# Kernel tuning notes

Hardware: AMD Instinct MI355X
Metric: run time of the kernel (lower is better)

The kernel has to match this reference:

```python
import jax, jax.numpy as jnp
import numpy as np

B, N, C, Cn, M = 4, 4096, 32, 64, 64


def fps(event, npoint):
    """Farthest point sampling, faithful to farthest_point_sample_batch.
    Returns selected points in ORIGINAL index order (masked_select semantics).
    event: [B, n, c] -> [B, npoint, c]
    """
    b, n, c = event.shape
    bidx = jnp.arange(b)
    barycenter = jnp.mean(event, axis=1, keepdims=True)            # [B,1,c]
    d0 = jnp.sum((event - barycenter) ** 2, axis=-1)               # [B,n]
    farthest = jnp.argmax(d0, axis=1)                              # [B]
    distance = jnp.full((b, n), 1e10, dtype=event.dtype)
    sel = jnp.zeros((b, n), dtype=bool)

    def body(carry, _):
        distance, farthest, sel = carry
        sel = sel.at[bidx, farthest].set(True)
        centroid = jnp.take_along_axis(event, farthest[:, None, None], axis=1)  # [B,1,c]
        d = jnp.sum((event - centroid) ** 2, axis=-1)              # [B,n]
        distance = jnp.minimum(distance, d)
        farthest = jnp.argmax(distance, axis=1)
        return (distance, farthest, sel), None

    (distance, farthest, sel), _ = jax.lax.scan(
        body, (distance, farthest, sel), None, length=npoint)
    # masked_select keeps original index order: stable sort puts selected first
    order = jnp.argsort(~sel, axis=1, stable=True)[:, :npoint]     # [B,npoint]
    return jnp.take_along_axis(event, order[:, :, None], axis=1)   # [B,npoint,c]


def setup_inputs() -> dict:
    key = jax.random.key(0)
    ks = jax.random.split(key, 7)
    s = 0.1
    return {
        "events_feature": jax.random.normal(ks[0], (B, N, C), jnp.float32),
        "W_qs": jax.random.normal(ks[1], (Cn, C), jnp.float32) * s,
        "W_ks": jax.random.normal(ks[2], (Cn, C), jnp.float32) * s,
        "W_vs": jax.random.normal(ks[3], (Cn, C), jnp.float32) * s,
        "W_pe": jax.random.normal(ks[4], (Cn, C), jnp.float32) * s,
        "W_sa1": jax.random.normal(ks[5], (1, Cn), jnp.float32) * s,
        "W_sa2": jax.random.normal(ks[6], (C, Cn), jnp.float32) * s,
    }


def reference(events_feature, W_qs, W_ks, W_vs, W_pe, W_sa1, W_sa2):
    q = events_feature @ W_qs.T                                   # [B,N,Cn]
    k = events_feature @ W_ks.T                                   # [B,N,Cn]
    v = events_feature @ W_vs.T                                   # [B,N,Cn]

    # position encoding: pairwise diff to M FPS-sampled events, then C->Cn
    ev_m = fps(events_feature, M)                                 # [B,M,C]
    pe = events_feature[:, :, None, :] - ev_m[:, None, :, :]      # [B,N,M,C]
    pe = pe @ W_pe.T                                              # [B,N,M,Cn]

    k_m = fps(k, M)                                               # [B,M,Cn]
    v_m = fps(v, M)                                               # [B,M,Cn]

    # vector attention scores: (q - k_m + pe) -> scalar per (n,m)
    sa = q[:, :, None, :] - k_m[:, None, :, :] + pe               # [B,N,M,Cn]
    logits = jnp.squeeze(sa @ W_sa1.T, -1)                        # [B,N,M]
    scores = jax.nn.softmax(logits, axis=-1)                      # [B,N,M]

    # Original: matmul(scores[B,1,N,M], (v_multi+pe).permute->[B,Cn,M,N]) then
    # sum over last axis. Summing first over n' is the same math and avoids the
    # [B,Cn,N,N] intermediate: sum_{n'} v_multi = N * v_m; sum_{n'} pe.
    S = N * v_m + jnp.sum(pe, axis=1)                             # [B,M,Cn]
    attn = jnp.einsum('bnm,bmc->bnc', scores, S)                  # [B,N,Cn]
    return attn @ W_sa2.T                                         # [B,N,C]
```

## Files before the change

kernel.cpp:

```cpp
#include <hip/hip_runtime.h>

constexpr int N_ = 4096, C_ = 32, CN_ = 64, M_ = 64;
constexpr int TPB = 1024;
constexpr int RPT = 3, LPT = 1;
constexpr int NREG = RPT * TPB;
constexpr int NLDS = N_ - NREG;
constexpr int NWAVES = TPB / 64;
constexpr int NTPB = 256;
constexpr int NCHUNK = N_ / NTPB;

__device__ __forceinline__ void pkfma(float2& a, float x0, float x1,
                                      float y0, float y1) {
  a.x = fmaf(x0, y0, a.x);
  a.y = fmaf(x1, y1, a.y);
}

__device__ __forceinline__ unsigned long long shfl_xor_u64(unsigned long long v, int m) {
  unsigned lo = __shfl_xor((unsigned)v, m);
  unsigned hi = __shfl_xor((unsigned)(v >> 32), m);
  return ((unsigned long long)hi << 32) | lo;
}

__device__ __forceinline__ unsigned fmap(float v) {
  unsigned u = __float_as_uint(v);
  u ^= (unsigned)((int)u >> 31) | 0x80000000u;
  return u;
}

__device__ __forceinline__ float rfl(float v) {
  return __uint_as_float(__builtin_amdgcn_readfirstlane(__float_as_uint(v)));
}

__global__ __launch_bounds__(NTPB, 1) void norms_kernel(
    const float* __restrict__ ev, const float* __restrict__ Wk,
    const float* __restrict__ Wv, float* __restrict__ nrm_all,
    float* __restrict__ zall, float* __restrict__ partials) {
  int blk = blockIdx.x;
  int chunk = blk & (NCHUNK - 1), br = blk >> 4;
  int r = br % 3, b = br / 3;
  int t = threadIdx.x;
  __shared__ float G[C_][C_ + 1];
  const float* W = (r == 1) ? Wk : Wv;
  for (int e = t; e < C_ * C_; e += NTPB) {
    int a = e >> 5, d = e & 31;
    float g;
    if (r == 0) {
      g = (a == d) ? 1.f : 0.f;
    } else {
      double acc = 0.0;
      for (int q = 0; q < CN_; ++q)
        acc += (double)W[q * C_ + a] * (double)W[q * C_ + d];
      g = (float)acc;
    }
    G[a][d] = g;
  }
  __syncthreads();
  int p = chunk * NTPB + t;
  const float4* row = (const float4*)(ev + ((size_t)b * N_ + p) * C_);
  float x[C_];
#pragma unroll
  for (int q = 0; q < C_ / 4; ++q) {
    float4 v = row[q];
    x[q * 4 + 0] = v.x; x[q * 4 + 1] = v.y; x[q * 4 + 2] = v.z; x[q * 4 + 3] = v.w;
  }
  double n = 0.0;
  float z[C_];
#pragma unroll
  for (int a = 0; a < C_; ++a) {
    double ta = 0.0;
#pragma unroll
    for (int d = 0; d < C_; ++d) ta += (double)G[a][d] * (double)x[d];
    z[a] = (float)ta;
    n += ta * (double)x[a];
  }
  nrm_all[(size_t)br * N_ + p] = (float)n;
  float4* zrow = (float4*)(zall + ((size_t)br * N_ + p) * C_);
#pragma unroll
  for (int q = 0; q < C_ / 4; ++q)
    zrow[q] = make_float4(z[q * 4 + 0], z[q * 4 + 1], z[q * 4 + 2], z[q * 4 + 3]);

  if (r == 0) {
    __shared__ float msum[NTPB / 64][C_];
#pragma unroll
    for (int d = 0; d < C_; ++d) {
      float s = x[d];
#pragma unroll
      for (int off = 32; off; off >>= 1) s += __shfl_xor(s, off);
      if ((t & 63) == 0) msum[t >> 6][d] = s;
    }
    __syncthreads();
    if (t < C_)
      partials[((size_t)b * NCHUNK + chunk) * C_ + t] =
          msum[0][t] + msum[1][t] + msum[2][t] + msum[3][t];
  }
}

__global__ __launch_bounds__(TPB, 1) void fps_kernel(
    const float* __restrict__ ev, const float* __restrict__ nrm_all,
    const float* __restrict__ zall, const float* __restrict__ partials,
    int* __restrict__ idx_ws) {
  const int t = threadIdx.x;
  const int blk = blockIdx.x;
  const int b = blk / 3;
  const float* evb = ev + (size_t)b * N_ * C_;
  const float* nrm = nrm_all + (size_t)blk * N_;
  const float4* zb4 = (const float4*)(zall + (size_t)blk * N_ * C_);

  __shared__ float LP[C_ / 4][NLDS][4];
  __shared__ float cf0[C_];
  __shared__ unsigned long long redK[2][NWAVES];

  float z[RPT][C_], pn[RPT], dmin[RPT];
  float nl, dminL;

#pragma unroll
  for (int j = 0; j < RPT; ++j) {
    int p = j * TPB + t;
#pragma unroll
    for (int q = 0; q < C_ / 4; ++q) {
      float4 v = zb4[(size_t)p * 8 + q];
      z[j][q * 4 + 0] = v.x; z[j][q * 4 + 1] = v.y;
      z[j][q * 4 + 2] = v.z; z[j][q * 4 + 3] = v.w;
    }
    pn[j] = nrm[p];
    dmin[j] = 1e10f;
  }
  {
    int p = NREG + t;
#pragma unroll
    for (int q = 0; q < C_ / 4; ++q) {
      float4 v = zb4[(size_t)p * 8 + q];
      *(float4*)&LP[q][t][0] = v;
    }
    nl = nrm[p];
    dminL = 1e10f;
  }
  if (t < C_) {
    float s = 0.f;
#pragma unroll
    for (int c = 0; c < NCHUNK; ++c) s += partials[((size_t)b * NCHUNK + c) * C_ + t];
    cf0[t] = s * (1.f / (float)N_);
  }
  __syncthreads();

  auto eval = [&](const float (&cs)[C_], float curN,
                  bool update) -> unsigned long long {
    float2 a2[RPT], aL;
#pragma unroll
    for (int j = 0; j < RPT; ++j) a2[j] = make_float2(0.f, 0.f);
    aL = make_float2(0.f, 0.f);
#pragma unroll
    for (int q = 0; q < C_ / 4; ++q) {
#pragma unroll
      for (int j = 0; j < RPT; ++j) {
        pkfma(a2[j], z[j][q * 4 + 0], z[j][q * 4 + 1], cs[q * 4 + 0], cs[q * 4 + 1]);
        pkfma(a2[j], z[j][q * 4 + 2], z[j][q * 4 + 3], cs[q * 4 + 2], cs[q * 4 + 3]);
      }
      float4 l = *(const float4*)&LP[q][t][0];
      pkfma(aL, l.x, l.y, cs[q * 4 + 0], cs[q * 4 + 1]);
      pkfma(aL, l.z, l.w, cs[q * 4 + 2], cs[q * 4 + 3]);
    }
    float bv = -3e38f; int bi = 0;
#pragma unroll
    for (int j = 0; j < RPT; ++j) {
      float acc = a2[j].x + a2[j].y;
      float d = fmaf(-2.f, acc, pn[j]) + curN;
      float v;
      if (update) { dmin[j] = fminf(dmin[j], d); v = dmin[j]; }
      else v = d;
      if (v > bv) { bv = v; bi = j * TPB + t; }
    }
    {
      float acc = aL.x + aL.y;
      float d = fmaf(-2.f, acc, nl) + curN;
      float v;
      if (update) { dminL = fminf(dminL, d); v = dminL; }
      else v = d;
      if (v > bv) { bv = v; bi = NREG + t; }
    }
    unsigned long long k =
        ((unsigned long long)fmap(bv) << 12) | (unsigned)(4095 - bi);
#pragma unroll
    for (int off = 1; off < 64; off <<= 1) {
      unsigned long long ko = shfl_xor_u64(k, off);
      if (ko > k) k = ko;
    }
    return k;
  };

  {
    float cs[C_];
#pragma unroll
    for (int d = 0; d < C_; ++d) cs[d] = rfl(cf0[d]);
    unsigned long long k = eval(cs, 0.f, false);
    if ((t & 63) == 0) redK[0][t >> 6] = k;
  }
  __syncthreads();

  for (int it = 0; it < M_; ++it) {
    int rb = it & 1;
    unsigned long long k = redK[rb][0];
#pragma unroll
    for (int w = 1; w < NWAVES; ++w) {
      unsigned long long kw = redK[rb][w];
      if (kw > k) k = kw;
    }
    int jsel = 4095 - (int)(k & 4095ull);
    if (t == 0) idx_ws[blk * M_ + it] = jsel;
    if (jsel < NREG) {
      if ((jsel & (TPB - 1)) == t) {
        int j = jsel >> 10;
        if (j == 0) dmin[0] = -3e38f;
        else if (j == 1) dmin[1] = -3e38f;
        else dmin[2] = -3e38f;
      }
    } else {
      if (jsel - NREG == t) dminL = -3e38f;
    }
    if (it == M_ - 1) break;
    int jsu = __builtin_amdgcn_readfirstlane(jsel);
    float curN = rfl(nrm[jsu]);
    const float* cf = evb + (size_t)jsu * C_;
    float cs[C_];
#pragma unroll
    for (int d = 0; d < C_; ++d) cs[d] = rfl(cf[d]);
    unsigned long long kk = eval(cs, curN, true);
    if ((t & 63) == 0) redK[rb ^ 1][t >> 6] = kk;
    __syncthreads();
  }
}

__global__ __launch_bounds__(256, 1) void finalize_kernel(
    const float* __restrict__ ev, const float* __restrict__ Wk,
    const float* __restrict__ Wv, const float* __restrict__ Wpe,
    const float* __restrict__ Wsa1, const float* __restrict__ Wsa2,
    const int* __restrict__ idx_ws, const float* __restrict__ partials,
    float* __restrict__ outvec_ws) {
  const int b = blockIdx.x;
  const int t = threadIdx.x;
  const float* evb = ev + (size_t)b * N_ * C_;

  __shared__ float Wl[3][CN_][C_];
  __shared__ float W1l[CN_];
  __shared__ float W2l[C_][CN_ + 1];
  __shared__ int   lidx[3][M_], sidx[3][M_];
  __shared__ float XP[3][M_][C_];
  __shared__ float PRJ[3][M_][CN_ + 1];
  __shared__ float sumx[C_], Pl[CN_], sl[M_], TP[4][CN_];

  {
    const float* Ws[3] = {Wpe, Wk, Wv};
#pragma unroll
    for (int r = 0; r < 3; ++r)
      for (int i = t; i < CN_ * C_ / 4; i += 256)
        ((float4*)&Wl[r][0][0])[i] = ((const float4*)Ws[r])[i];
    if (t < CN_) W1l[t] = Wsa1[t];
    for (int i = t; i < C_ * CN_; i += 256)
      W2l[i >> 6][i & 63] = Wsa2[i];
  }
  if (t < 192) {
    int r = t >> 6, mm = t & 63;
    lidx[r][mm] = idx_ws[(b * 3 + r) * M_ + mm];
  }
  if (t < C_) {
    float s = 0.f;
#pragma unroll
    for (int c = 0; c < NCHUNK; ++c) s += partials[((size_t)b * NCHUNK + c) * C_ + t];
    sumx[t] = s;
  }
  __syncthreads();
  if (t < 192) {
    int r = t >> 6, mm = t & 63;
    int my = lidx[r][mm];
    int rank = 0;
#pragma unroll
    for (int j = 0; j < M_; ++j)
      rank += (lidx[r][j] < my) || (lidx[r][j] == my && j < mm);
    sidx[r][rank] = my;
  }
  __syncthreads();
  for (int g = t; g < 3 * M_ * 8; g += 256) {
    int row = g >> 3, q = g & 7;
    int r = row >> 6, m = row & 63;
    int pi = sidx[r][m];
    *(float4*)&XP[r][m][q * 4] = ((const float4*)(evb + (size_t)pi * C_))[q];
  }
  __syncthreads();
  {
    int w = t >> 6, cn = t & 63;
    if (w < 3) {
      float wr[C_];
#pragma unroll
      for (int q = 0; q < C_ / 4; ++q) {
        float4 v = *(const float4*)&Wl[w][cn][q * 4];
        wr[q * 4 + 0] = v.x; wr[q * 4 + 1] = v.y;
        wr[q * 4 + 2] = v.z; wr[q * 4 + 3] = v.w;
      }
      for (int m = 0; m < M_; ++m) {
        float2 a = make_float2(0.f, 0.f);
#pragma unroll
        for (int q = 0; q < C_ / 4; ++q) {
          float4 x = *(const float4*)&XP[w][m][q * 4];
          pkfma(a, x.x, x.y, wr[q * 4 + 0], wr[q * 4 + 1]);
          pkfma(a, x.z, x.w, wr[q * 4 + 2], wr[q * 4 + 3]);
        }
        PRJ[w][m][cn] = a.x + a.y;
      }
    } else {
      float a = 0.f;
#pragma unroll
      for (int c = 0; c < C_; ++c) a = fmaf(sumx[c], Wl[0][cn][c], a);
      Pl[cn] = a;
    }
  }
  __syncthreads();
  if (t < 64) {
    float cm = 0.f;
#pragma unroll 8
    for (int cn = 0; cn < CN_; ++cn)
      cm = fmaf(PRJ[1][t][cn] + PRJ[0][t][cn], W1l[cn], cm);
    float lg = -cm;
    float mx = lg;
#pragma unroll
    for (int off = 32; off; off >>= 1) mx = fmaxf(mx, __shfl_xor(mx, off));
    float e = expf(lg - mx);
    float ssum = e;
#pragma unroll
    for (int off = 32; off; off >>= 1) ssum += __shfl_xor(ssum, off);
    sl[t] = e / ssum;
  }
  __syncthreads();
  {
    int cn = t & 63, h = t >> 6;
    float a = 0.f;
#pragma unroll
    for (int i = 0; i < 16; ++i) {
      int mm = h * 16 + i;
      a = fmaf(sl[mm],
               fmaf((float)N_, PRJ[2][mm][cn], Pl[cn]) - (float)N_ * PRJ[0][mm][cn],
               a);
    }
    TP[h][cn] = a;
  }
  __syncthreads();
  if (t < C_) {
    float o = 0.f;
#pragma unroll 8
    for (int cn = 0; cn < CN_; ++cn) {
      float tv = TP[0][cn] + TP[1][cn] + TP[2][cn] + TP[3][cn];
      o = fmaf(tv, W2l[t][cn], o);
    }
    outvec_ws[b * C_ + t] = o;
  }
}

__global__ void bcast_kernel(const float* __restrict__ outvec_ws,
                             float4* __restrict__ out) {
  int i = blockIdx.x * 256 + threadIdx.x;
  int b = i >> 15;
  int j = i & 7;
  const float4* ov = (const float4*)outvec_ws;
  out[i] = ov[b * 8 + j];
}

extern "C" void kernel_launch(void* const* d_in, const int* in_sizes, int n_in,
                              void* d_out, int out_size, void* d_ws, size_t ws_size,
                              hipStream_t stream) {
  const float* ev   = (const float*)d_in[0];
  const float* Wk   = (const float*)d_in[2];
  const float* Wv   = (const float*)d_in[3];
  const float* Wpe  = (const float*)d_in[4];
  const float* Wsa1 = (const float*)d_in[5];
  const float* Wsa2 = (const float*)d_in[6];
  float* out = (float*)d_out;

  char* ws = (char*)d_ws;
  int*   idx    = (int*)ws;
  float* parts  = (float*)(ws + 3072);
  float* outvec = (float*)(ws + 11264);
  float* nrm    = (float*)(ws + 11776);
  float* zall   = (float*)(ws + 208384);

  norms_kernel   <<<dim3(192), dim3(NTPB), 0, stream>>>(ev, Wk, Wv, nrm, zall, parts);
  fps_kernel     <<<dim3(12),  dim3(TPB),  0, stream>>>(ev, nrm, zall, parts, idx);
  finalize_kernel<<<dim3(4),   dim3(256),  0, stream>>>(ev, Wk, Wv, Wpe, Wsa1, Wsa2,
                                                        idx, parts, outvec);
  bcast_kernel   <<<dim3(512), dim3(256),  0, stream>>>(outvec, (float4*)out);
}
```

Baseline: 193.7 us.

## Use scalar FMA chains, shuffle-based cross-wave max, and explicit waves-per-EU attributes

Replaces the paired float2 accumulators in the FPS distance evaluation and in the projection loop with single scalar FMA chains, which removes the final pair-add and may change register pressure. The serial 16-entry scan of per-wave keys is replaced by each lane loading one entry and doing a 4-step xor-shuffle max reduction. Launch bounds are swapped for amdgpu_flat_work_group_size and amdgpu_waves_per_eu attributes to steer register allocation. The single accumulator chains lengthen the dependency chain and slightly change floating-point summation order, so argmax ties could shift.

```diff
diff --git a/kernel.cpp b/kernel.cpp
--- a/kernel.cpp
+++ b/kernel.cpp
@@ -9,12 +9,6 @@
 constexpr int NTPB = 256;
 constexpr int NCHUNK = N_ / NTPB;
 
-__device__ __forceinline__ void pkfma(float2& a, float x0, float x1,
-                                      float y0, float y1) {
-  a.x = fmaf(x0, y0, a.x);
-  a.y = fmaf(x1, y1, a.y);
-}
-
 __device__ __forceinline__ unsigned long long shfl_xor_u64(unsigned long long v, int m) {
   unsigned lo = __shfl_xor((unsigned)v, m);
   unsigned hi = __shfl_xor((unsigned)(v >> 32), m);
@@ -31,7 +25,9 @@
   return __uint_as_float(__builtin_amdgcn_readfirstlane(__float_as_uint(v)));
 }
 
-__global__ __launch_bounds__(NTPB, 1) void norms_kernel(
+__global__ __attribute__((amdgpu_flat_work_group_size(NTPB, NTPB),
+                          amdgpu_waves_per_eu(1, 4)))
+void norms_kernel(
     const float* __restrict__ ev, const float* __restrict__ Wk,
     const float* __restrict__ Wv, float* __restrict__ nrm_all,
     float* __restrict__ zall, float* __restrict__ partials) {
@@ -95,7 +91,9 @@
   }
 }
 
-__global__ __launch_bounds__(TPB, 1) void fps_kernel(
+__global__ __attribute__((amdgpu_flat_work_group_size(TPB, TPB),
+                          amdgpu_waves_per_eu(4, 4)))
+void fps_kernel(
     const float* __restrict__ ev, const float* __restrict__ nrm_all,
     const float* __restrict__ zall, const float* __restrict__ partials,
     int* __restrict__ idx_ws) {
@@ -145,34 +143,31 @@
 
   auto eval = [&](const float (&cs)[C_], float curN,
                   bool update) -> unsigned long long {
-    float2 a2[RPT], aL;
-#pragma unroll
-    for (int j = 0; j < RPT; ++j) a2[j] = make_float2(0.f, 0.f);
-    aL = make_float2(0.f, 0.f);
+    float a0 = 0.f, a1 = 0.f, a2 = 0.f, aL = 0.f;
 #pragma unroll
     for (int q = 0; q < C_ / 4; ++q) {
-#pragma unroll
-      for (int j = 0; j < RPT; ++j) {
-        pkfma(a2[j], z[j][q * 4 + 0], z[j][q * 4 + 1], cs[q * 4 + 0], cs[q * 4 + 1]);
-        pkfma(a2[j], z[j][q * 4 + 2], z[j][q * 4 + 3], cs[q * 4 + 2], cs[q * 4 + 3]);
+      float4 l = *(const float4*)&LP[q][t][0];
+#pragma unroll
+      for (int e = 0; e < 4; ++e) {
+        float c = cs[q * 4 + e];
+        a0 = fmaf(z[0][q * 4 + e], c, a0);
+        a1 = fmaf(z[1][q * 4 + e], c, a1);
+        a2 = fmaf(z[2][q * 4 + e], c, a2);
+        aL = fmaf((&l.x)[e], c, aL);
       }
-      float4 l = *(const float4*)&LP[q][t][0];
-      pkfma(aL, l.x, l.y, cs[q * 4 + 0], cs[q * 4 + 1]);
-      pkfma(aL, l.z, l.w, cs[q * 4 + 2], cs[q * 4 + 3]);
-    }
+    }
+    float acc[RPT] = {a0, a1, a2};
     float bv = -3e38f; int bi = 0;
 #pragma unroll
     for (int j = 0; j < RPT; ++j) {
-      float acc = a2[j].x + a2[j].y;
-      float d = fmaf(-2.f, acc, pn[j]) + curN;
+      float d = fmaf(-2.f, acc[j], pn[j]) + curN;
       float v;
       if (update) { dmin[j] = fminf(dmin[j], d); v = dmin[j]; }
       else v = d;
       if (v > bv) { bv = v; bi = j * TPB + t; }
     }
     {
-      float acc = aL.x + aL.y;
-      float d = fmaf(-2.f, acc, nl) + curN;
+      float d = fmaf(-2.f, aL, nl) + curN;
       float v;
       if (update) { dminL = fminf(dminL, d); v = dminL; }
       else v = d;
@@ -199,11 +194,11 @@
 
   for (int it = 0; it < M_; ++it) {
     int rb = it & 1;
-    unsigned long long k = redK[rb][0];
-#pragma unroll
-    for (int w = 1; w < NWAVES; ++w) {
-      unsigned long long kw = redK[rb][w];
-      if (kw > k) k = kw;
+    unsigned long long k = redK[rb][t & (NWAVES - 1)];
+#pragma unroll
+    for (int off = 1; off < NWAVES; off <<= 1) {
+      unsigned long long ko = shfl_xor_u64(k, off);
+      if (ko > k) k = ko;
     }
     int jsel = 4095 - (int)(k & 4095ull);
     if (t == 0) idx_ws[blk * M_ + it] = jsel;
@@ -297,14 +292,16 @@
         wr[q * 4 + 2] = v.z; wr[q * 4 + 3] = v.w;
       }
       for (int m = 0; m < M_; ++m) {
-        float2 a = make_float2(0.f, 0.f);
+        float a = 0.f;
 #pragma unroll
         for (int q = 0; q < C_ / 4; ++q) {
           float4 x = *(const float4*)&XP[w][m][q * 4];
-          pkfma(a, x.x, x.y, wr[q * 4 + 0], wr[q * 4 + 1]);
-          pkfma(a, x.z, x.w, wr[q * 4 + 2], wr[q * 4 + 3]);
+          a = fmaf(x.x, wr[q * 4 + 0], a);
+          a = fmaf(x.y, wr[q * 4 + 1], a);
+          a = fmaf(x.z, wr[q * 4 + 2], a);
+          a = fmaf(x.w, wr[q * 4 + 3], a);
         }
-        PRJ[w][m][cn] = a.x + a.y;
+        PRJ[w][m][cn] = a;
       }
     } else {
       float a = 0.f;
```

Result: no change. 194.7 us (+0.5%).
